# Kernel tuning notes

Hardware: AMD Instinct MI355X
Metric: run time of the kernel (lower is better)

## Reference

```python
import jax, jax.numpy as jnp
import numpy as np

N, E, D, L = 50000, 800000, 128, 3

def setup_inputs() -> dict:
    key = jax.random.key(0)
    ks = jax.random.split(key, 6)
    X = jax.random.normal(ks[0], (N, D), dtype=jnp.float32)
    edge_index = jax.random.randint(ks[1], (2, E), 0, N, dtype=jnp.int64)
    eps = jax.random.normal(ks[2], (L,), dtype=jnp.float32)
    # Glorot-ish scaling for stability
    W1 = jax.random.normal(ks[3], (L, D, D), dtype=jnp.float32) / np.sqrt(D)
    b1 = jnp.zeros((L, D), dtype=jnp.float32)
    W2 = jax.random.normal(ks[4], (L, D, D), dtype=jnp.float32) / np.sqrt(D)
    b2 = jnp.zeros((L, D), dtype=jnp.float32)
    return {"X": X, "edge_index": edge_index, "eps": eps,
            "W1": W1, "b1": b1, "W2": W2, "b2": b2}

def reference(X, edge_index, eps, W1, b1, W2, b2):
    src = edge_index[0]  # message sources j (flow source_to_target)
    dst = edge_index[1]  # aggregation targets i
    n = X.shape[0]
    for i in range(L):  # fixed small layer loop
        X0 = X
        # propagate: gather X_j over edges, scatter-add to targets
        S = jax.ops.segment_sum(X[src], dst, num_segments=n)  # [N, D]
        Z = (1.0 + eps[i]) * X + S
        # MLP: Linear -> ReLU -> Linear
        H = jnp.maximum(Z @ W1[i] + b1[i], 0.0)
        X = H @ W2[i] + b2[i]
        X = X + X0  # residual=True
    return X
```

## Files before the change

kernel.cpp:

```cpp
#include <hip/hip_runtime.h>

#define NN 50000
#define NE 800000
#define DD 128
#define NL 3
#define ELLW 64
#define MT_TOTAL (NN / 16)
#define MT_PER_XCD 391
#define NODES_PER_XCD (MT_PER_XCD * 16)
#define SCAT_BLKS (MT_PER_XCD * 8)
#define SCAT_CHUNK 2048
#define PACK_BLKS ((6 * 2048 + 255) / 256)
#define INIT_BLKS 3128
#define NODE_BLKS ((NN + 255) / 256)

typedef short bf16x8 __attribute__((ext_vector_type(8)));
typedef float f32x4 __attribute__((ext_vector_type(4)));
typedef _Float16 half8 __attribute__((ext_vector_type(8)));
typedef unsigned short u16x8 __attribute__((ext_vector_type(8)));

__device__ __forceinline__ unsigned short f2bf(float x) {
  unsigned u = __float_as_uint(x);
  u += 0x7FFFu + ((u >> 16) & 1u);
  return (unsigned short)(u >> 16);
}
__device__ __forceinline__ float bf2f(unsigned short h) {
  return __uint_as_float(((unsigned)h) << 16);
}
__device__ __forceinline__ void cvt8(const float* zz, bf16x8* hi, bf16x8* lo) {
#pragma unroll
  for (int i = 0; i < 8; ++i) {
    unsigned short h = f2bf(zz[i]);
    (*hi)[i] = (short)h;
    (*lo)[i] = (short)f2bf(zz[i] - bf2f(h));
  }
}

__global__ __launch_bounds__(256) void prologue_k(
    const int* __restrict__ ei, int* __restrict__ cnt, unsigned short* __restrict__ ell,
    const float* __restrict__ W1, const float* __restrict__ W2,
    unsigned short* __restrict__ Wp,
    const float* __restrict__ X, _Float16* __restrict__ Xh)
{
  int b = blockIdx.x;
  if (b < SCAT_BLKS) {
    int g = b & 7, chunk = b >> 3;
    int lo = g * NODES_PER_XCD, hi = lo + NODES_PER_XCD;
    int base = chunk * SCAT_CHUNK + threadIdx.x * 8;
    if (base + 7 < NE) {
      int4 d0 = *(const int4*)(ei + NE + base);
      int4 d1 = *(const int4*)(ei + NE + base + 4);
      int4 s0 = *(const int4*)(ei + base);
      int4 s1 = *(const int4*)(ei + base + 4);
      int dd[8] = {d0.x, d0.y, d0.z, d0.w, d1.x, d1.y, d1.z, d1.w};
      int ss[8] = {s0.x, s0.y, s0.z, s0.w, s1.x, s1.y, s1.z, s1.w};
#pragma unroll
      for (int i = 0; i < 8; ++i) {
        int d = dd[i];
        if (d >= lo && d < hi) {
          int pos = atomicAdd(&cnt[d], 1);
          if (pos < ELLW) ell[(size_t)d * ELLW + pos] = (unsigned short)ss[i];
        }
      }
    } else {
      for (int e = base; e < NE; ++e) {
        int d = ei[NE + e];
        if (d >= lo && d < hi) {
          int pos = atomicAdd(&cnt[d], 1);
          if (pos < ELLW) ell[(size_t)d * ELLW + pos] = (unsigned short)ei[e];
        }
      }
    }
  } else if (b < SCAT_BLKS + PACK_BLKS) {
    int t = (b - SCAT_BLKS) * 256 + threadIdx.x;
    if (t < 6 * 2048) {
      int m = t >> 11;
      int rem = t & 2047;
      int l = rem & 63;
      int ntks = rem >> 6;
      int ks = ntks & 3, nt = ntks >> 2;
      const float* W = (m < 3) ? (W1 + (size_t)m * DD * DD) : (W2 + (size_t)(m - 3) * DD * DD);
      int col = nt * 16 + (l & 15);
      int k0 = ks * 32 + (l >> 4) * 8;
      unsigned short* hi = Wp + (size_t)m * 2 * DD * DD + (size_t)rem * 8;
      unsigned short* lo = hi + DD * DD;
#pragma unroll
      for (int i = 0; i < 8; ++i) {
        float w = W[(size_t)(k0 + i) * DD + col];
        unsigned short h = f2bf(w);
        hi[i] = h;
        lo[i] = f2bf(w - bf2f(h));
      }
    }
  } else {
    int bb = b - SCAT_BLKS - PACK_BLKS;
    int g = bb & 7, ii = bb >> 3;
    int mt = g * MT_PER_XCD + ii;
    if (mt < MT_TOTAL) {
      size_t base = (size_t)mt * 16 * DD + threadIdx.x * 8;
      const float4* p = (const float4*)(X + base);
      float4 a = p[0], bb2 = p[1];
      half8 h;
      h[0] = (_Float16)a.x;   h[1] = (_Float16)a.y;   h[2] = (_Float16)a.z;   h[3] = (_Float16)a.w;
      h[4] = (_Float16)bb2.x; h[5] = (_Float16)bb2.y; h[6] = (_Float16)bb2.z; h[7] = (_Float16)bb2.w;
      *(half8*)(Xh + base) = h;
    }
  }
}

__global__ __launch_bounds__(256) void hist_k(const int* __restrict__ cnt,
                                              int* __restrict__ hist) {
  __shared__ int lh[8 * 65];
  for (int i = threadIdx.x; i < 8 * 65; i += 256) lh[i] = 0;
  __syncthreads();
  int n = blockIdx.x * 256 + threadIdx.x;
  if (n < NN) {
    int deg = cnt[n]; deg = deg > ELLW ? ELLW : deg;
    int part = n / NODES_PER_XCD;
    atomicAdd(&lh[part * 65 + deg], 1);
  }
  __syncthreads();
  for (int i = threadIdx.x; i < 8 * 65; i += 256)
    if (lh[i]) atomicAdd(&hist[i], lh[i]);
}

__global__ __launch_bounds__(64) void prefix_k(const int* __restrict__ hist,
                                               int* __restrict__ cursor) {
  int g = threadIdx.x;
  if (g < 8) {
    int base = g * NODES_PER_XCD;
    for (int b = 0; b <= ELLW; ++b) { cursor[g * 65 + b] = base; base += hist[g * 65 + b]; }
  }
}

__global__ __launch_bounds__(256) void place_k(const int* __restrict__ cnt,
                                               int* __restrict__ cursor,
                                               int* __restrict__ perm) {
  int n = blockIdx.x * 256 + threadIdx.x;
  if (n >= NN) return;
  int deg = cnt[n]; deg = deg > ELLW ? ELLW : deg;
  int part = n / NODES_PER_XCD;
  int rank = atomicAdd(&cursor[part * 65 + deg], 1);
  perm[rank] = n | (deg << 16);
}

template<int OUT_F32>
__global__ __launch_bounds__(256) void fused_layer_k(
    const _Float16* __restrict__ Xh_in,
    const int* __restrict__ perm, const unsigned short* __restrict__ ell,
    const float* __restrict__ eps, int layer,
    const unsigned short* __restrict__ Wp1, const float* __restrict__ b1,
    const unsigned short* __restrict__ Wp2, const float* __restrict__ b2,
    float* __restrict__ Xf_out, _Float16* __restrict__ Xh_out)
{
  __shared__ float ztile[16 * 132];
  __shared__ unsigned short rtile[16 * 136];
  const int mt = (blockIdx.x & 7) * MT_PER_XCD + (blockIdx.x >> 3);
  if (mt >= MT_TOTAL) return;
  const int w = threadIdx.x >> 6, l = threadIdx.x & 63;
  const int c = l & 15, grp = l >> 4;

  {
    const float e1 = 1.0f + eps[layer];
    const int nl = w * 4 + grp;
    const int pe = perm[mt * 16 + nl];
    const int node = pe & 0xFFFF;
    const int deg = pe >> 16;
    const unsigned short* el = ell + (size_t)node * ELLW;
    const u16x8* el8 = (const u16x8*)el;
    half8 sv = *(const half8*)(Xh_in + (size_t)node * DD + c * 8);
    *(u16x8*)(rtile + nl * 136 + c * 8) = *(const u16x8*)&sv;
    half8 acch = (half8)(_Float16)0.0f;
    int nf8 = deg >> 3;
    u16x8 nxt;
    if (nf8) nxt = el8[0];
    for (int t = 0; t < nf8; ++t) {
      u16x8 cur = nxt;
      if (t + 1 < nf8) nxt = el8[t + 1];
      half8 v0 = *(const half8*)(Xh_in + (size_t)cur[0] * DD + c * 8);
      half8 v1 = *(const half8*)(Xh_in + (size_t)cur[1] * DD + c * 8);
      half8 v2 = *(const half8*)(Xh_in + (size_t)cur[2] * DD + c * 8);
      half8 v3 = *(const half8*)(Xh_in + (size_t)cur[3] * DD + c * 8);
      half8 v4 = *(const half8*)(Xh_in + (size_t)cur[4] * DD + c * 8);
      half8 v5 = *(const half8*)(Xh_in + (size_t)cur[5] * DD + c * 8);
      half8 v6 = *(const half8*)(Xh_in + (size_t)cur[6] * DD + c * 8);
      half8 v7 = *(const half8*)(Xh_in + (size_t)cur[7] * DD + c * 8);
      half8 s = ((v0 + v1) + (v2 + v3)) + ((v4 + v5) + (v6 + v7));
      acch += s;
    }
    for (int j = nf8 * 8; j < deg; ++j) {
      half8 v = *(const half8*)(Xh_in + (size_t)el[j] * DD + c * 8);
      acch += v;
    }
    float acc[8];
#pragma unroll
    for (int i = 0; i < 8; ++i) acc[i] = fmaf(e1, (float)sv[i], (float)acch[i]);
    float* dst = ztile + nl * 132 + c * 8;
    *(float4*)dst = make_float4(acc[0], acc[1], acc[2], acc[3]);
    *(float4*)(dst + 4) = make_float4(acc[4], acc[5], acc[6], acc[7]);
  }
  __syncthreads();

  f32x4 acc1[2];
#pragma unroll
  for (int nt = 0; nt < 2; ++nt) acc1[nt] = (f32x4){0.f, 0.f, 0.f, 0.f};
  {
    const float* arow = ztile + (l & 15) * 132;
    const unsigned short* Whi = Wp1;
    const unsigned short* Wlo = Wp1 + DD * DD;
#pragma unroll
    for (int ks = 0; ks < 4; ++ks) {
      const float* zp = arow + ks * 32 + grp * 8;
      float zz[8] = {zp[0], zp[1], zp[2], zp[3], zp[4], zp[5], zp[6], zp[7]};
      bf16x8 ahi, alo; cvt8(zz, &ahi, &alo);
#pragma unroll
      for (int nt = 0; nt < 2; ++nt) {
        int ntb = w * 2 + nt;
        size_t off = ((size_t)(ntb * 4 + ks) * 64 + l) * 8;
        bf16x8 bhi = *(const bf16x8*)(Whi + off);
        bf16x8 blo = *(const bf16x8*)(Wlo + off);
        acc1[nt] = __builtin_amdgcn_mfma_f32_16x16x32_bf16(ahi, bhi, acc1[nt], 0, 0, 0);
        acc1[nt] = __builtin_amdgcn_mfma_f32_16x16x32_bf16(ahi, blo, acc1[nt], 0, 0, 0);
        acc1[nt] = __builtin_amdgcn_mfma_f32_16x16x32_bf16(alo, bhi, acc1[nt], 0, 0, 0);
      }
    }
  }
  __syncthreads();

  {
#pragma unroll
    for (int nt = 0; nt < 2; ++nt) {
      int ntb = w * 2 + nt;
      float bv = b1[ntb * 16 + c];
#pragma unroll
      for (int r = 0; r < 4; ++r)
        ztile[(grp * 4 + r) * 132 + ntb * 16 + c] = fmaxf(acc1[nt][r] + bv, 0.f);
    }
  }
  __syncthreads();

  f32x4 acc2[2];
#pragma unroll
  for (int nt = 0; nt < 2; ++nt) acc2[nt] = (f32x4){0.f, 0.f, 0.f, 0.f};
  {
    const float* arow = ztile + (l & 15) * 132;
    const unsigned short* Whi = Wp2;
    const unsigned short* Wlo = Wp2 + DD * DD;
#pragma unroll
    for (int ks = 0; ks < 4; ++ks) {
      const float* hp = arow + ks * 32 + grp * 8;
      float hh[8] = {hp[0], hp[1], hp[2], hp[3], hp[4], hp[5], hp[6], hp[7]};
      bf16x8 ahi, alo; cvt8(hh, &ahi, &alo);
#pragma unroll
      for (int nt = 0; nt < 2; ++nt) {
        int ntb = w * 2 + nt;
        size_t off = ((size_t)(ntb * 4 + ks) * 64 + l) * 8;
        bf16x8 bhi = *(const bf16x8*)(Whi + off);
        bf16x8 blo = *(const bf16x8*)(Wlo + off);
        acc2[nt] = __builtin_amdgcn_mfma_f32_16x16x32_bf16(ahi, bhi, acc2[nt], 0, 0, 0);
        acc2[nt] = __builtin_amdgcn_mfma_f32_16x16x32_bf16(ahi, blo, acc2[nt], 0, 0, 0);
        acc2[nt] = __builtin_amdgcn_mfma_f32_16x16x32_bf16(alo, bhi, acc2[nt], 0, 0, 0);
      }
    }
#pragma unroll
    for (int nt = 0; nt < 2; ++nt) {
      int ntb = w * 2 + nt;
      int col = ntb * 16 + c;
      float bv = b2[col];
#pragma unroll
      for (int r = 0; r < 4; ++r) {
        int row = grp * 4 + r;
        int onode = perm[mt * 16 + row] & 0xFFFF;
        size_t idx = (size_t)onode * DD + col;
        unsigned short rb = rtile[row * 136 + col];
        float rv = (float)(*(_Float16*)&rb);
        float v = acc2[nt][r] + bv + rv;
        if (OUT_F32) Xf_out[idx] = v;
        else         Xh_out[idx] = (_Float16)v;
      }
    }
  }
}

extern "C" void kernel_launch(void* const* d_in, const int* in_sizes, int n_in,
                              void* d_out, int out_size, void* d_ws, size_t ws_size,
                              hipStream_t stream) {
  const float* X   = (const float*)d_in[0];
  const int*   ei  = (const int*)d_in[1];
  const float* eps = (const float*)d_in[2];
  const float* W1  = (const float*)d_in[3];
  const float* b1  = (const float*)d_in[4];
  const float* W2  = (const float*)d_in[5];
  const float* b2  = (const float*)d_in[6];
  float* Xout = (float*)d_out;

  char* ws = (char*)d_ws;
  size_t off = 0;
  int* cnt    = (int*)(ws + off); off += 256 * (((size_t)NN * 4 + 255) / 256);
  int* hist   = (int*)(ws + off); off += 256 * ((8 * 65 * 4 + 255) / 256);
  size_t zero_bytes = off;
  int* cursor = (int*)(ws + off); off += 256 * ((8 * 65 * 4 + 255) / 256);
  int* perm   = (int*)(ws + off); off += 256 * (((size_t)(MT_PER_XCD * 8 * 16) * 4 + 255) / 256);
  unsigned short* ell = (unsigned short*)(ws + off); off += (size_t)NN * ELLW * 2;
  unsigned short* Wp  = (unsigned short*)(ws + off); off += (size_t)6 * 2 * DD * DD * 2;
  off = 256 * ((off + 255) / 256);
  _Float16* Xh0 = (_Float16*)(ws + off); off += (size_t)NN * DD * 2;
  _Float16* Xh1 = (_Float16*)(ws + off); off += (size_t)NN * DD * 2;

  hipMemsetAsync(cnt, 0, zero_bytes, stream);
  prologue_k<<<SCAT_BLKS + PACK_BLKS + INIT_BLKS, 256, 0, stream>>>(
      ei, cnt, ell, W1, W2, Wp, X, Xh0);
  hist_k<<<NODE_BLKS, 256, 0, stream>>>(cnt, hist);
  prefix_k<<<1, 64, 0, stream>>>(hist, cursor);
  place_k<<<NODE_BLKS, 256, 0, stream>>>(cnt, cursor, perm);

  const int fgrid = MT_PER_XCD * 8;
  fused_layer_k<0><<<fgrid, 256, 0, stream>>>(Xh0, perm, ell, eps, 0,
      Wp + (size_t)0 * 2 * DD * DD, b1 + 0 * DD,
      Wp + (size_t)3 * 2 * DD * DD, b2 + 0 * DD, nullptr, Xh1);
  fused_layer_k<0><<<fgrid, 256, 0, stream>>>(Xh1, perm, ell, eps, 1,
      Wp + (size_t)1 * 2 * DD * DD, b1 + 1 * DD,
      Wp + (size_t)4 * 2 * DD * DD, b2 + 1 * DD, nullptr, Xh0);
  fused_layer_k<1><<<fgrid, 256, 0, stream>>>(Xh0, perm, ell, eps, 2,
      Wp + (size_t)2 * 2 * DD * DD, b1 + 2 * DD,
      Wp + (size_t)5 * 2 * DD * DD, b2 + 2 * DD, Xout, nullptr);
}
```

Baseline: 196.8 us.

## Merge degree sort into one per-partition kernel and stride tile order

Replaces the three-kernel histogram/prefix/place sequence with a single 8-block kernel in which each block bins its XCD partition's nodes by degree using shared-memory counters and a serial prefix. This removes two kernel launches and the global atomics on the histogram and cursor arrays. In exchange, only 8 blocks process all 50k nodes, so that stage has very little parallelism. The fused layer kernel also visits tiles within each partition in a stride-7 order instead of sequentially, which interleaves degree classes across concurrently running blocks to even out load.

```diff
diff --git a/kernel.cpp b/kernel.cpp
--- a/kernel.cpp
+++ b/kernel.cpp
@@ -12,7 +12,6 @@
 #define SCAT_CHUNK 2048
 #define PACK_BLKS ((6 * 2048 + 255) / 256)
 #define INIT_BLKS 3128
-#define NODE_BLKS ((NN + 255) / 256)
 
 typedef short bf16x8 __attribute__((ext_vector_type(8)));
 typedef float f32x4 __attribute__((ext_vector_type(4)));
@@ -108,40 +107,30 @@
   }
 }
 
-__global__ __launch_bounds__(256) void hist_k(const int* __restrict__ cnt,
-                                              int* __restrict__ hist) {
-  __shared__ int lh[8 * 65];
-  for (int i = threadIdx.x; i < 8 * 65; i += 256) lh[i] = 0;
-  __syncthreads();
-  int n = blockIdx.x * 256 + threadIdx.x;
-  if (n < NN) {
+__global__ __launch_bounds__(256) void sort_k(const int* __restrict__ cnt,
+                                              int* __restrict__ perm) {
+  __shared__ int lh[ELLW + 1];
+  __shared__ int cur[ELLW + 1];
+  int g = blockIdx.x;
+  int base = g * NODES_PER_XCD;
+  int nend = base + NODES_PER_XCD; if (nend > NN) nend = NN;
+  for (int i = threadIdx.x; i <= ELLW; i += 256) lh[i] = 0;
+  __syncthreads();
+  for (int n = base + threadIdx.x; n < nend; n += 256) {
     int deg = cnt[n]; deg = deg > ELLW ? ELLW : deg;
-    int part = n / NODES_PER_XCD;
-    atomicAdd(&lh[part * 65 + deg], 1);
-  }
-  __syncthreads();
-  for (int i = threadIdx.x; i < 8 * 65; i += 256)
-    if (lh[i]) atomicAdd(&hist[i], lh[i]);
-}
-
-__global__ __launch_bounds__(64) void prefix_k(const int* __restrict__ hist,
-                                               int* __restrict__ cursor) {
-  int g = threadIdx.x;
-  if (g < 8) {
-    int base = g * NODES_PER_XCD;
-    for (int b = 0; b <= ELLW; ++b) { cursor[g * 65 + b] = base; base += hist[g * 65 + b]; }
-  }
-}
-
-__global__ __launch_bounds__(256) void place_k(const int* __restrict__ cnt,
-                                               int* __restrict__ cursor,
-                                               int* __restrict__ perm) {
-  int n = blockIdx.x * 256 + threadIdx.x;
-  if (n >= NN) return;
-  int deg = cnt[n]; deg = deg > ELLW ? ELLW : deg;
-  int part = n / NODES_PER_XCD;
-  int rank = atomicAdd(&cursor[part * 65 + deg], 1);
-  perm[rank] = n | (deg << 16);
+    atomicAdd(&lh[deg], 1);
+  }
+  __syncthreads();
+  if (threadIdx.x == 0) {
+    int run = base;
+    for (int b = 0; b <= ELLW; ++b) { cur[b] = run; run += lh[b]; }
+  }
+  __syncthreads();
+  for (int n = base + threadIdx.x; n < nend; n += 256) {
+    int deg = cnt[n]; deg = deg > ELLW ? ELLW : deg;
+    int rank = atomicAdd(&cur[deg], 1);
+    perm[rank] = n | (deg << 16);
+  }
 }
 
 template<int OUT_F32>
@@ -155,7 +144,10 @@
 {
   __shared__ float ztile[16 * 132];
   __shared__ unsigned short rtile[16 * 136];
-  const int mt = (blockIdx.x & 7) * MT_PER_XCD + (blockIdx.x >> 3);
+  const int part = blockIdx.x & 7;
+  const int ii = blockIdx.x >> 3;
+  const int iis = (ii * 7) % MT_PER_XCD;
+  const int mt = part * MT_PER_XCD + iis;
   if (mt >= MT_TOTAL) return;
   const int w = threadIdx.x >> 6, l = threadIdx.x & 63;
   const int c = l & 15, grp = l >> 4;
@@ -296,23 +288,18 @@
 
   char* ws = (char*)d_ws;
   size_t off = 0;
-  int* cnt    = (int*)(ws + off); off += 256 * (((size_t)NN * 4 + 255) / 256);
-  int* hist   = (int*)(ws + off); off += 256 * ((8 * 65 * 4 + 255) / 256);
-  size_t zero_bytes = off;
-  int* cursor = (int*)(ws + off); off += 256 * ((8 * 65 * 4 + 255) / 256);
-  int* perm   = (int*)(ws + off); off += 256 * (((size_t)(MT_PER_XCD * 8 * 16) * 4 + 255) / 256);
+  int* cnt  = (int*)(ws + off); off += 256 * (((size_t)NN * 4 + 255) / 256);
+  int* perm = (int*)(ws + off); off += 256 * (((size_t)(MT_PER_XCD * 8 * 16) * 4 + 255) / 256);
   unsigned short* ell = (unsigned short*)(ws + off); off += (size_t)NN * ELLW * 2;
   unsigned short* Wp  = (unsigned short*)(ws + off); off += (size_t)6 * 2 * DD * DD * 2;
   off = 256 * ((off + 255) / 256);
   _Float16* Xh0 = (_Float16*)(ws + off); off += (size_t)NN * DD * 2;
   _Float16* Xh1 = (_Float16*)(ws + off); off += (size_t)NN * DD * 2;
 
-  hipMemsetAsync(cnt, 0, zero_bytes, stream);
+  hipMemsetAsync(cnt, 0, (size_t)NN * 4, stream);
   prologue_k<<<SCAT_BLKS + PACK_BLKS + INIT_BLKS, 256, 0, stream>>>(
       ei, cnt, ell, W1, W2, Wp, X, Xh0);
-  hist_k<<<NODE_BLKS, 256, 0, stream>>>(cnt, hist);
-  prefix_k<<<1, 64, 0, stream>>>(hist, cursor);
-  place_k<<<NODE_BLKS, 256, 0, stream>>>(cnt, cursor, perm);
+  sort_k<<<8, 256, 0, stream>>>(cnt, perm);
 
   const int fgrid = MT_PER_XCD * 8;
   fused_layer_k<0><<<fgrid, 256, 0, stream>>>(Xh0, perm, ell, eps, 0,
```

Result: faster. 186.8 us, median of 2 (-5.1%).
